# Kernel optimization log

Hardware: AMD Instinct MI355X
Metric: run time of the kernel (lower is better)

## Reference

```python
import jax, jax.numpy as jnp
import numpy as np

BN_EPS = 1e-5      # torch BatchNorm2d default eps
NORM_EPS = 1e-12   # torch F.normalize default eps


def conv1x1_bn(x, W, b, gamma, beta, mean, var):
    # 1x1 conv == channel matmul; BN in eval mode (running stats)
    y = jnp.einsum('oc,nchw->nohw', W, x) + b[None, :, None, None]
    scale = gamma / jnp.sqrt(var + BN_EPS)
    shift = beta - mean * scale
    return y * scale[None, :, None, None] + shift[None, :, None, None]


def _l2norm(x, axis):
    n = jnp.sqrt(jnp.sum(x * x, axis=axis, keepdims=True))
    return x / jnp.maximum(n, NORM_EPS)


def setup_inputs() -> dict:
    key = jax.random.key(0)
    ks = jax.random.split(key, 16)
    N, C, H, W = 16, 64, 256, 256
    QK = 32
    d = {}
    d['x'] = jax.random.normal(ks[0], (N, C, H, W), jnp.float32)
    # Q projection (C -> 32) + BN
    d['Wq'] = jax.random.normal(ks[1], (QK, C), jnp.float32) * (1.0 / np.sqrt(C))
    d['bq'] = jax.random.normal(ks[2], (QK,), jnp.float32) * 0.01
    d['q_gamma'] = jnp.ones((QK,), jnp.float32)
    d['q_beta'] = jnp.zeros((QK,), jnp.float32)
    d['q_mean'] = jax.random.normal(ks[3], (QK,), jnp.float32) * 0.1
    d['q_var'] = jax.random.uniform(ks[4], (QK,), jnp.float32, 0.5, 1.5)
    # K projection (C -> 32) + BN
    d['Wk'] = jax.random.normal(ks[5], (QK, C), jnp.float32) * (1.0 / np.sqrt(C))
    d['bk'] = jax.random.normal(ks[6], (QK,), jnp.float32) * 0.01
    d['k_gamma'] = jnp.ones((QK,), jnp.float32)
    d['k_beta'] = jnp.zeros((QK,), jnp.float32)
    d['k_mean'] = jax.random.normal(ks[7], (QK,), jnp.float32) * 0.1
    d['k_var'] = jax.random.uniform(ks[8], (QK,), jnp.float32, 0.5, 1.5)
    # V projection (C -> C) + BN
    d['Wv'] = jax.random.normal(ks[9], (C, C), jnp.float32) * (1.0 / np.sqrt(C))
    d['bv'] = jax.random.normal(ks[10], (C,), jnp.float32) * 0.01
    d['v_gamma'] = jnp.ones((C,), jnp.float32)
    d['v_beta'] = jnp.zeros((C,), jnp.float32)
    d['v_mean'] = jax.random.normal(ks[11], (C,), jnp.float32) * 0.1
    d['v_var'] = jax.random.uniform(ks[12], (C,), jnp.float32, 0.5, 1.5)
    # output conv-BN-ReLU (C -> C)
    d['Wo'] = jax.random.normal(ks[13], (C, C), jnp.float32) * (1.0 / np.sqrt(C))
    d['bo'] = jax.random.normal(ks[14], (C,), jnp.float32) * 0.01
    d['o_gamma'] = jnp.ones((C,), jnp.float32)
    d['o_beta'] = jnp.zeros((C,), jnp.float32)
    d['o_mean'] = jax.random.normal(ks[15], (C,), jnp.float32) * 0.1
    d['o_var'] = jax.random.uniform(jax.random.fold_in(key, 99), (C,), jnp.float32, 0.5, 1.5)
    return d


def reference(x, Wq, bq, q_gamma, q_beta, q_mean, q_var,
              Wk, bk, k_gamma, k_beta, k_mean, k_var,
              Wv, bv, v_gamma, v_beta, v_mean, v_var,
              Wo, bo, o_gamma, o_beta, o_mean, o_var):
    N, C, H, W = x.shape
    HW = H * W
    Qm = conv1x1_bn(x, Wq, bq, q_gamma, q_beta, q_mean, q_var)   # [N,32,H,W]
    Km = conv1x1_bn(x, Wk, bk, k_gamma, k_beta, k_mean, k_var)   # [N,32,H,W]
    V0 = conv1x1_bn(x, Wv, bv, v_gamma, v_beta, v_mean, v_var)   # [N,C,H,W]

    Q = jnp.transpose(Qm.reshape(N, 32, HW), (0, 2, 1))          # [N,HW,32]
    Q = _l2norm(Q, axis=2)
    K = _l2norm(Km.reshape(N, 32, HW), axis=1)                   # [N,32,HW]
    V = jax.nn.relu(jnp.transpose(V0.reshape(N, C, HW), (0, 2, 1)))  # [N,HW,C]

    f = jnp.einsum('nks,nsc->nkc', K, V)                         # [N,32,C]
    y = jnp.einsum('nsk,nkc->nsc', Q, f)                         # [N,HW,C]
    y = jnp.transpose(y, (0, 2, 1)).reshape(N, C, H, W)

    out = jax.nn.relu(conv1x1_bn(y, Wo, bo, o_gamma, o_beta, o_mean, o_var))
    return out + V0
```

## Files before the change

kernel.cpp:

```cpp
#include <hip/hip_runtime.h>

#define HW 65536
#define NBATCH 16
#define CCH 64
#define QKC 32

#define OFF_WQT 0
#define OFF_BQ  2048
#define OFF_WKT 2080
#define OFF_BK  4128
#define OFF_WVT 4160
#define OFF_BV  8256
#define OFF_WO  8320
#define OFF_BO  12416
#define OFF_F   12544
#define OFF_MT  45312

#define BPN_A 128
#define BPN_B 128

typedef __attribute__((ext_vector_type(4))) float f32x4;
typedef __attribute__((ext_vector_type(8))) short bf16x8;
typedef __attribute__((ext_vector_type(4))) short bf16x4;

#define MFMA_P(a, b, c) __builtin_amdgcn_mfma_f32_16x16x32_bf16(a, b, c, 0, 0, 0)
#define MFMA_O(a, b, c) __builtin_amdgcn_mfma_f32_16x16x16bf16_1k(a, b, c, 0, 0, 0)

__device__ __forceinline__ short f2bf(float f) {
    __bf16 h = (__bf16)f;
    return __builtin_bit_cast(short, h);
}

__global__ __launch_bounds__(256) void k0_fold(
    const float* __restrict__ Wq, const float* __restrict__ bq,
    const float* __restrict__ qg, const float* __restrict__ qb,
    const float* __restrict__ qm, const float* __restrict__ qv,
    const float* __restrict__ Wk, const float* __restrict__ bk,
    const float* __restrict__ kg, const float* __restrict__ kb,
    const float* __restrict__ km, const float* __restrict__ kvar,
    const float* __restrict__ Wv, const float* __restrict__ bv,
    const float* __restrict__ vg, const float* __restrict__ vb,
    const float* __restrict__ vm, const float* __restrict__ vvar,
    const float* __restrict__ Wo, const float* __restrict__ bo,
    const float* __restrict__ og, const float* __restrict__ ob,
    const float* __restrict__ om, const float* __restrict__ ovar,
    float* __restrict__ ws)
{
    const int idx = blockIdx.x * 256 + threadIdx.x;
    if (idx < 2048) {
        const int c = idx >> 5, i = idx & 31;
        const float s = qg[i] * rsqrtf(qv[i] + 1e-5f);
        ws[OFF_WQT + idx] = Wq[i * 64 + c] * s;
    } else if (idx < 2080) {
        const int i = idx - 2048;
        const float s = qg[i] * rsqrtf(qv[i] + 1e-5f);
        ws[OFF_BQ + i] = bq[i] * s + qb[i] - qm[i] * s;
    } else if (idx < 4128) {
        const int t = idx - 2080;
        const int c = t >> 5, i = t & 31;
        const float s = kg[i] * rsqrtf(kvar[i] + 1e-5f);
        ws[OFF_WKT + t] = Wk[i * 64 + c] * s;
    } else if (idx < 4160) {
        const int i = idx - 4128;
        const float s = kg[i] * rsqrtf(kvar[i] + 1e-5f);
        ws[OFF_BK + i] = bk[i] * s + kb[i] - km[i] * s;
    } else if (idx < 8256) {
        const int t = idx - 4160;
        const int c = t >> 6, o = t & 63;
        const float s = vg[o] * rsqrtf(vvar[o] + 1e-5f);
        ws[OFF_WVT + t] = Wv[o * 64 + c] * s;
    } else if (idx < 8320) {
        const int o = idx - 8256;
        const float s = vg[o] * rsqrtf(vvar[o] + 1e-5f);
        ws[OFF_BV + o] = bv[o] * s + vb[o] - vm[o] * s;
    } else if (idx < 12416) {
        const int t = idx - 8320;
        const int c = t >> 6, j = t & 63;
        const float s = og[c] * rsqrtf(ovar[c] + 1e-5f);
        ws[OFF_WO + t] = Wo[c * 64 + j] * s;
    } else if (idx < 12480) {
        const int c = idx - 12416;
        const float s = og[c] * rsqrtf(ovar[c] + 1e-5f);
        ws[OFF_BO + c] = bo[c] * s + ob[c] - om[c] * s;
    } else if (idx < 12480 + 32768) {
        ws[OFF_F + (idx - 12480)] = 0.0f;
    }
}

__global__ __launch_bounds__(256) void k1_passA(const float* __restrict__ x,
                                                const float* __restrict__ wsc,
                                                float* __restrict__ f)
{
    __shared__ float red[4 * 2048];

    const int tid = threadIdx.x;
    const int w = tid >> 6;
    const int lane = tid & 63;
    const int ln = lane & 15;
    const int lg = lane >> 4;

    const int n = blockIdx.x / BPN_A;
    const int bslot = blockIdx.x % BPN_A;
    const float* xn = x + (size_t)n * CCH * HW;

    bf16x8 wkf[2][2];
#pragma unroll
    for (int kk = 0; kk < 2; kk++)
#pragma unroll
        for (int t = 0; t < 2; t++) {
            bf16x8 a;
#pragma unroll
            for (int j = 0; j < 8; j++)
                a[j] = f2bf(wsc[OFF_WKT + (kk * 32 + lg * 8 + j) * 32 + t * 16 + ln]);
            wkf[kk][t] = a;
        }
    bf16x8 wvf[2][4];
#pragma unroll
    for (int kk = 0; kk < 2; kk++)
#pragma unroll
        for (int t = 0; t < 4; t++) {
            bf16x8 a;
#pragma unroll
            for (int j = 0; j < 8; j++)
                a[j] = f2bf(wsc[OFF_WVT + (kk * 32 + lg * 8 + j) * 64 + t * 16 + ln]);
            wvf[kk][t] = a;
        }
    float bkb[2], bvb[4];
#pragma unroll
    for (int t = 0; t < 2; t++) bkb[t] = wsc[OFF_BK + t * 16 + ln];
#pragma unroll
    for (int t = 0; t < 4; t++) bvb[t] = wsc[OFF_BV + t * 16 + ln];

    f32x4 facc[2][4];
#pragma unroll
    for (int t = 0; t < 2; t++)
#pragma unroll
        for (int vt = 0; vt < 4; vt++) facc[t][vt] = (f32x4){0.f, 0.f, 0.f, 0.f};

    for (int chunk = bslot; chunk < HW / 64; chunk += BPN_A) {
        const int sbase = chunk * 64 + w * 16;

        bf16x8 xa[2];
#pragma unroll
        for (int kk = 0; kk < 2; kk++) {
            const float* xp = xn + (kk * 32 + lg * 8) * HW + sbase + ln;
            bf16x8 a;
#pragma unroll
            for (int j = 0; j < 8; j++) a[j] = f2bf(xp[j * HW]);
            xa[kk] = a;
        }

        f32x4 dk[2], dv[4];
#pragma unroll
        for (int t = 0; t < 2; t++) dk[t] = (f32x4){bkb[t], bkb[t], bkb[t], bkb[t]};
#pragma unroll
        for (int t = 0; t < 4; t++) dv[t] = (f32x4){bvb[t], bvb[t], bvb[t], bvb[t]};
#pragma unroll
        for (int kk = 0; kk < 2; kk++) {
#pragma unroll
            for (int t = 0; t < 2; t++) dk[t] = MFMA_P(xa[kk], wkf[kk][t], dk[t]);
#pragma unroll
            for (int t = 0; t < 4; t++) dv[t] = MFMA_P(xa[kk], wvf[kk][t], dv[t]);
        }

        float inv[4];
#pragma unroll
        for (int r = 0; r < 4; r++) {
            float s = dk[0][r] * dk[0][r] + dk[1][r] * dk[1][r];
            s += __shfl_xor(s, 1, 64);
            s += __shfl_xor(s, 2, 64);
            s += __shfl_xor(s, 4, 64);
            s += __shfl_xor(s, 8, 64);
            inv[r] = 1.0f / fmaxf(sqrtf(s), 1e-12f);
        }

        bf16x4 ka[2], vb[4];
#pragma unroll
        for (int t = 0; t < 2; t++)
#pragma unroll
            for (int r = 0; r < 4; r++) ka[t][r] = f2bf(dk[t][r] * inv[r]);
#pragma unroll
        for (int t = 0; t < 4; t++)
#pragma unroll
            for (int r = 0; r < 4; r++) vb[t][r] = f2bf(fmaxf(dv[t][r], 0.0f));

#pragma unroll
        for (int t = 0; t < 2; t++)
#pragma unroll
            for (int vt = 0; vt < 4; vt++)
                facc[t][vt] = MFMA_O(ka[t], vb[vt], facc[t][vt]);
    }

#pragma unroll
    for (int t = 0; t < 2; t++)
#pragma unroll
        for (int vt = 0; vt < 4; vt++)
#pragma unroll
            for (int r = 0; r < 4; r++)
                red[w * 2048 + (t * 16 + lg * 4 + r) * 64 + vt * 16 + ln] = facc[t][vt][r];
    __syncthreads();
    float* fn = f + n * (QKC * CCH);
    for (int idx = tid; idx < 2048; idx += 256)
        atomicAdd(&fn[idx], red[idx] + red[2048 + idx] + red[4096 + idx] + red[6144 + idx]);
}

__global__ __launch_bounds__(256) void k2_M(const float* __restrict__ wsc,
                                            float* __restrict__ ws)
{
    const int idx = blockIdx.x * 256 + threadIdx.x;
    if (idx >= NBATCH * QKC * CCH) return;
    const int n = idx / (QKC * CCH);
    const int r = idx % (QKC * CCH);
    const int i = r >> 6, c = r & 63;
    const float* wo = wsc + OFF_WO + c * 64;
    const float* fr = wsc + OFF_F + n * 2048 + i * 64;
    float acc = 0.0f;
#pragma unroll
    for (int j = 0; j < 64; j++) acc += wo[j] * fr[j];
    ws[OFF_MT + idx] = acc;
}

__global__ __launch_bounds__(256) void k3_passB(const float* __restrict__ x,
                                               const float* __restrict__ wsc,
                                               float* __restrict__ out)
{
    __shared__ float qt[4][16 * 36];

    const int tid = threadIdx.x;
    const int w = tid >> 6;
    const int lane = tid & 63;
    const int ln = lane & 15;
    const int lg = lane >> 4;

    const int n = blockIdx.x / BPN_B;
    const int slot = blockIdx.x % BPN_B;
    const float* xn = x + (size_t)n * CCH * HW;
    float* on = out + (size_t)n * CCH * HW;

    bf16x8 wqf[2][2];
#pragma unroll
    for (int kk = 0; kk < 2; kk++)
#pragma unroll
        for (int t = 0; t < 2; t++) {
            bf16x8 a;
#pragma unroll
            for (int j = 0; j < 8; j++)
                a[j] = f2bf(wsc[OFF_WQT + (kk * 32 + lg * 8 + j) * 32 + t * 16 + ln]);
            wqf[kk][t] = a;
        }
    bf16x8 wvf[2][4];
#pragma unroll
    for (int kk = 0; kk < 2; kk++)
#pragma unroll
        for (int t = 0; t < 4; t++) {
            bf16x8 a;
#pragma unroll
            for (int j = 0; j < 8; j++)
                a[j] = f2bf(wsc[OFF_WVT + (kk * 32 + lg * 8 + j) * 64 + t * 16 + ln]);
            wvf[kk][t] = a;
        }
    bf16x8 mtf[4];
#pragma unroll
    for (int t = 0; t < 4; t++) {
        bf16x8 a;
#pragma unroll
        for (int j = 0; j < 8; j++)
            a[j] = f2bf(wsc[OFF_MT + n * 2048 + (lg * 8 + j) * 64 + t * 16 + ln]);
        mtf[t] = a;
    }
    float bqb[2], bvb[4], bob[4];
#pragma unroll
    for (int t = 0; t < 2; t++) bqb[t] = wsc[OFF_BQ + t * 16 + ln];
#pragma unroll
    for (int t = 0; t < 4; t++) bvb[t] = wsc[OFF_BV + t * 16 + ln];
#pragma unroll
    for (int t = 0; t < 4; t++) bob[t] = wsc[OFF_BO + t * 16 + ln];

    for (int chunk = slot; chunk < HW / 64; chunk += BPN_B) {
        const int sbase = chunk * 64 + w * 16;

        bf16x8 xa[2];
#pragma unroll
        for (int kk = 0; kk < 2; kk++) {
            const float* xp = xn + (kk * 32 + lg * 8) * HW + sbase + ln;
            bf16x8 a;
#pragma unroll
            for (int j = 0; j < 8; j++) a[j] = f2bf(xp[j * HW]);
            xa[kk] = a;
        }

        f32x4 dq[2], dv0[4];
#pragma unroll
        for (int t = 0; t < 2; t++) dq[t] = (f32x4){bqb[t], bqb[t], bqb[t], bqb[t]};
#pragma unroll
        for (int t = 0; t < 4; t++) dv0[t] = (f32x4){bvb[t], bvb[t], bvb[t], bvb[t]};
#pragma unroll
        for (int kk = 0; kk < 2; kk++) {
#pragma unroll
            for (int t = 0; t < 2; t++) dq[t] = MFMA_P(xa[kk], wqf[kk][t], dq[t]);
#pragma unroll
            for (int t = 0; t < 4; t++) dv0[t] = MFMA_P(xa[kk], wvf[kk][t], dv0[t]);
        }

        float inv[4];
#pragma unroll
        for (int r = 0; r < 4; r++) {
            float s = dq[0][r] * dq[0][r] + dq[1][r] * dq[1][r];
            s += __shfl_xor(s, 1, 64);
            s += __shfl_xor(s, 2, 64);
            s += __shfl_xor(s, 4, 64);
            s += __shfl_xor(s, 8, 64);
            inv[r] = 1.0f / fmaxf(sqrtf(s), 1e-12f);
        }

#pragma unroll
        for (int t = 0; t < 2; t++)
#pragma unroll
            for (int r = 0; r < 4; r++)
                qt[w][(lg * 4 + r) * 36 + t * 16 + ln] = dq[t][r] * inv[r];
        const f32x4 qlo = *(const f32x4*)&qt[w][ln * 36 + lg * 8];
        const f32x4 qhi = *(const f32x4*)&qt[w][ln * 36 + lg * 8 + 4];
        bf16x8 aq;
#pragma unroll
        for (int j = 0; j < 4; j++) { aq[j] = f2bf(qlo[j]); aq[4 + j] = f2bf(qhi[j]); }

        f32x4 dy[4];
#pragma unroll
        for (int t = 0; t < 4; t++) dy[t] = (f32x4){bob[t], bob[t], bob[t], bob[t]};
#pragma unroll
        for (int t = 0; t < 4; t++) dy[t] = MFMA_P(aq, mtf[t], dy[t]);

#pragma unroll
        for (int t = 0; t < 4; t++) {
            float* op = on + (size_t)(t * 16 + ln) * HW + sbase + lg * 4;
            f32x4 o4;
#pragma unroll
            for (int r = 0; r < 4; r++)
                o4[r] = fmaxf(dy[t][r], 0.0f) + dv0[t][r];
            __builtin_nontemporal_store(o4, (f32x4*)op);
        }
    }
}

extern "C" void kernel_launch(void* const* d_in, const int* in_sizes, int n_in,
                              void* d_out, int out_size, void* d_ws, size_t ws_size,
                              hipStream_t stream)
{
    const float* x    = (const float*)d_in[0];
    const float* Wq   = (const float*)d_in[1];
    const float* bq   = (const float*)d_in[2];
    const float* qg   = (const float*)d_in[3];
    const float* qb   = (const float*)d_in[4];
    const float* qm   = (const float*)d_in[5];
    const float* qv   = (const float*)d_in[6];
    const float* Wk   = (const float*)d_in[7];
    const float* bk   = (const float*)d_in[8];
    const float* kg   = (const float*)d_in[9];
    const float* kb   = (const float*)d_in[10];
    const float* km   = (const float*)d_in[11];
    const float* kvar = (const float*)d_in[12];
    const float* Wv   = (const float*)d_in[13];
    const float* bv   = (const float*)d_in[14];
    const float* vg   = (const float*)d_in[15];
    const float* vb   = (const float*)d_in[16];
    const float* vm   = (const float*)d_in[17];
    const float* vvar = (const float*)d_in[18];
    const float* Wo   = (const float*)d_in[19];
    const float* bo   = (const float*)d_in[20];
    const float* og   = (const float*)d_in[21];
    const float* ob   = (const float*)d_in[22];
    const float* om   = (const float*)d_in[23];
    const float* ovar = (const float*)d_in[24];

    float* ws  = (float*)d_ws;
    float* out = (float*)d_out;

    k0_fold<<<177, 256, 0, stream>>>(Wq, bq, qg, qb, qm, qv,
                                     Wk, bk, kg, kb, km, kvar,
                                     Wv, bv, vg, vb, vm, vvar,
                                     Wo, bo, og, ob, om, ovar, ws);

    k1_passA<<<NBATCH * BPN_A, 256, 0, stream>>>(x, (const float*)ws, ws + OFF_F);

    k2_M<<<128, 256, 0, stream>>>((const float*)ws, ws);

    k3_passB<<<NBATCH * BPN_B, 256, 0, stream>>>(x, (const float*)ws, out);
}
```

Measured before the change: 214.7 us.

## Software-pipeline x loads in both passes and reverse chunk order in second pass

Both the f-accumulation kernel and the output kernel now prefetch the next chunk's 16 x values into registers while computing the current chunk, with a fixed, fully unrolled iteration count. The output kernel also walks its chunks in reverse order, so it starts on the data the first pass touched last, which may still be in L2/MALL cache. This is meant to hide global load latency and reuse cached x between the two passes, at the cost of more registers and larger unrolled code.

```diff
diff --git a/kernel.cpp b/kernel.cpp
--- a/kernel.cpp
+++ b/kernel.cpp
@@ -18,6 +18,8 @@
 
 #define BPN_A 128
 #define BPN_B 128
+#define NIT_A ((HW / 64) / BPN_A)
+#define NIT_B ((HW / 64) / BPN_B)
 
 typedef __attribute__((ext_vector_type(4))) float f32x4;
 typedef __attribute__((ext_vector_type(8))) short bf16x8;
@@ -137,18 +139,35 @@
 #pragma unroll
         for (int vt = 0; vt < 4; vt++) facc[t][vt] = (f32x4){0.f, 0.f, 0.f, 0.f};
 
-    for (int chunk = bslot; chunk < HW / 64; chunk += BPN_A) {
-        const int sbase = chunk * 64 + w * 16;
+    float xf[16];
+    {
+        const int sbase = bslot * 64 + w * 16;
+#pragma unroll
+        for (int kk = 0; kk < 2; kk++) {
+            const float* xp = xn + (size_t)(kk * 32 + lg * 8) * HW + sbase + ln;
+#pragma unroll
+            for (int j = 0; j < 8; j++) xf[kk * 8 + j] = xp[j * HW];
+        }
+    }
+
+#pragma unroll
+    for (int it = 0; it < NIT_A; ++it) {
+        float xf2[16];
+        if (it + 1 < NIT_A) {
+            const int sb2 = (bslot + (it + 1) * BPN_A) * 64 + w * 16;
+#pragma unroll
+            for (int kk = 0; kk < 2; kk++) {
+                const float* xp = xn + (size_t)(kk * 32 + lg * 8) * HW + sb2 + ln;
+#pragma unroll
+                for (int j = 0; j < 8; j++) xf2[kk * 8 + j] = xp[j * HW];
+            }
+        }
 
         bf16x8 xa[2];
 #pragma unroll
-        for (int kk = 0; kk < 2; kk++) {
-            const float* xp = xn + (kk * 32 + lg * 8) * HW + sbase + ln;
-            bf16x8 a;
-#pragma unroll
-            for (int j = 0; j < 8; j++) a[j] = f2bf(xp[j * HW]);
-            xa[kk] = a;
-        }
+        for (int kk = 0; kk < 2; kk++)
+#pragma unroll
+            for (int j = 0; j < 8; j++) xa[kk][j] = f2bf(xf[kk * 8 + j]);
 
         f32x4 dk[2], dv[4];
 #pragma unroll
@@ -189,6 +208,11 @@
 #pragma unroll
             for (int vt = 0; vt < 4; vt++)
                 facc[t][vt] = MFMA_O(ka[t], vb[vt], facc[t][vt]);
+
+        if (it + 1 < NIT_A) {
+#pragma unroll
+            for (int i = 0; i < 16; i++) xf[i] = xf2[i];
+        }
     }
 
 #pragma unroll
@@ -276,18 +300,39 @@
 #pragma unroll
     for (int t = 0; t < 4; t++) bob[t] = wsc[OFF_BO + t * 16 + ln];
 
-    for (int chunk = slot; chunk < HW / 64; chunk += BPN_B) {
-        const int sbase = chunk * 64 + w * 16;
+    const int c0 = (HW / 64) - 1 - slot;
+
+    float xf[16];
+    {
+        const int sbase = c0 * 64 + w * 16;
+#pragma unroll
+        for (int kk = 0; kk < 2; kk++) {
+            const float* xp = xn + (size_t)(kk * 32 + lg * 8) * HW + sbase + ln;
+#pragma unroll
+            for (int j = 0; j < 8; j++) xf[kk * 8 + j] = xp[j * HW];
+        }
+    }
+
+#pragma unroll
+    for (int it = 0; it < NIT_B; ++it) {
+        const int sbase = (c0 - it * BPN_B) * 64 + w * 16;
+
+        float xf2[16];
+        if (it + 1 < NIT_B) {
+            const int sb2 = (c0 - (it + 1) * BPN_B) * 64 + w * 16;
+#pragma unroll
+            for (int kk = 0; kk < 2; kk++) {
+                const float* xp = xn + (size_t)(kk * 32 + lg * 8) * HW + sb2 + ln;
+#pragma unroll
+                for (int j = 0; j < 8; j++) xf2[kk * 8 + j] = xp[j * HW];
+            }
+        }
 
         bf16x8 xa[2];
 #pragma unroll
-        for (int kk = 0; kk < 2; kk++) {
-            const float* xp = xn + (kk * 32 + lg * 8) * HW + sbase + ln;
-            bf16x8 a;
-#pragma unroll
-            for (int j = 0; j < 8; j++) a[j] = f2bf(xp[j * HW]);
-            xa[kk] = a;
-        }
+        for (int kk = 0; kk < 2; kk++)
+#pragma unroll
+            for (int j = 0; j < 8; j++) xa[kk][j] = f2bf(xf[kk * 8 + j]);
 
         f32x4 dq[2], dv0[4];
 #pragma unroll
@@ -338,6 +383,11 @@
             for (int r = 0; r < 4; r++)
                 o4[r] = fmaxf(dy[t][r], 0.0f) + dv0[t][r];
             __builtin_nontemporal_store(o4, (f32x4*)op);
+        }
+
+        if (it + 1 < NIT_B) {
+#pragma unroll
+            for (int i = 0; i < 16; i++) xf[i] = xf2[i];
         }
     }
 }
```

New measurement: 201.0 us. 6.4% less time.
